# Performance work log

Measured on AMD Instinct MI355X. Metric: run time of the kernel, lower is better.

Reference implementation:

```python
import jax, jax.numpy as jnp
import numpy as np

N_NODES = 50000
N_EDGES = 600000
IN_FEAT = 128
EDGE_DIM = 3
N_HEADS = 4
OUT_FEAT = 32  # per head; N_HEADS*OUT_FEAT == IN_FEAT -> residual_proj is Identity


def setup_inputs() -> dict:
    key = jax.random.key(0)
    ks = jax.random.split(key, 16)
    s = 0.05
    H, F = N_HEADS, OUT_FEAT
    return {
        "node_feats": jax.random.normal(ks[0], (N_NODES, IN_FEAT), jnp.float32),
        "edge_feat": jax.random.normal(ks[1], (N_EDGES, EDGE_DIM), jnp.float32),
        "src": jax.random.randint(ks[2], (N_EDGES,), 0, N_NODES),
        "dst": jax.random.randint(ks[3], (N_EDGES,), 0, N_NODES),
        "W_em1": jax.random.normal(ks[4], (EDGE_DIM, 2 * EDGE_DIM), jnp.float32) * s,
        "b_em1": jnp.zeros((2 * EDGE_DIM,), jnp.float32),
        "W_em2": jax.random.normal(ks[5], (2 * EDGE_DIM, EDGE_DIM), jnp.float32) * s,
        "b_em2": jnp.zeros((EDGE_DIM,), jnp.float32),
        "W_np": jax.random.normal(ks[6], (IN_FEAT, IN_FEAT), jnp.float32) * s,
        "b_np": jnp.zeros((IN_FEAT,), jnp.float32),
        "W_fc": jax.random.normal(ks[7], (IN_FEAT + EDGE_DIM, H * F), jnp.float32) * s,
        "attn_l": jax.random.normal(ks[8], (H, F), jnp.float32) * s,
        "attn_r": jax.random.normal(ks[9], (H, F), jnp.float32) * s,
        "gat_bias": jnp.zeros((H * F,), jnp.float32),
        "ln_gamma": jnp.ones((H * F,), jnp.float32),
        "ln_beta": jnp.zeros((H * F,), jnp.float32),
    }


def reference(node_feats, edge_feat, src, dst, W_em1, b_em1, W_em2, b_em2,
              W_np, b_np, W_fc, attn_l, attn_r, gat_bias, ln_gamma, ln_beta):
    N = node_feats.shape[0]
    H, F = attn_l.shape
    # edge MLP: Linear -> SiLU -> Linear
    e = jax.nn.silu(edge_feat @ W_em1 + b_em1) @ W_em2 + b_em2            # [E, ED]
    p = node_feats @ W_np + b_np                                          # [N, IN]
    src_in = jnp.concatenate([p[src], e], axis=1)                         # [E, IN+ED]
    dst_in = jnp.concatenate([p[dst], e], axis=1)                         # [E, IN+ED]
    temp = jnp.zeros((N, src_in.shape[1]), node_feats.dtype)
    temp = temp.at[src].add(src_in).at[dst].add(dst_in)                   # scatter_add x2
    # GATConv (eval mode: feat_drop/attn_drop are identity)
    h = (temp @ W_fc).reshape(N, H, F)                                    # [N, H, F]
    el = jnp.einsum('nhf,hf->nh', h, attn_l)                              # [N, H]
    er = jnp.einsum('nhf,hf->nh', h, attn_r)                              # [N, H]
    logits = jax.nn.leaky_relu(el[src] + er[dst], negative_slope=0.2)     # [E, H]
    # destination-wise edge softmax (stable)
    m = jax.ops.segment_max(logits, dst, num_segments=N)                  # [N, H]
    a = jnp.exp(logits - m[dst])                                          # [E, H]
    z = jax.ops.segment_sum(a, dst, num_segments=N)                       # [N, H]
    alpha = a / z[dst]                                                    # [E, H]
    msg = alpha[:, :, None] * h[src]                                      # [E, H, F]
    rst = jax.ops.segment_sum(msg, dst, num_segments=N)                   # [N, H, F]
    rst = rst + gat_bias.reshape(1, H, F)
    gat_out = rst.reshape(N, H * F)
    out = gat_out + node_feats                                            # residual (Identity proj)
    mu = out.mean(axis=-1, keepdims=True)
    var = out.var(axis=-1, keepdims=True)
    out = (out - mu) / jnp.sqrt(var + 1e-5) * ln_gamma + ln_beta          # LayerNorm
    return jax.nn.silu(out)
```

## Files before the change

kernel.cpp:

```cpp
#include <hip/hip_runtime.h>
#include <hip/hip_bf16.h>

#define IN_FEAT 128
#define N_HEADS 4
#define OUT_FEAT 32

typedef __attribute__((ext_vector_type(8))) short short8;
typedef __attribute__((ext_vector_type(4))) float floatx4;

__device__ __forceinline__ void bf16split(float x, short& hi, short& lo) {
    unsigned u = __float_as_uint(x);
    unsigned r = (u + 0x7FFFu + ((u >> 16) & 1u)) & 0xFFFF0000u;
    hi = (short)(r >> 16);
    float res = x - __uint_as_float(r);
    unsigned u2 = __float_as_uint(res);
    unsigned r2 = u2 + 0x7FFFu + ((u2 >> 16) & 1u);
    lo = (short)(r2 >> 16);
}

__device__ __forceinline__ unsigned short bf16rne(float x) {
    unsigned u = __float_as_uint(x);
    return (unsigned short)((u + 0x7FFFu + ((u >> 16) & 1u)) >> 16);
}

__global__ void edge_scatter_kernel(const float* __restrict__ ef,
                                    const int* __restrict__ src, const int* __restrict__ dst,
                                    const float* __restrict__ W1, const float* __restrict__ b1,
                                    const float* __restrict__ W2, const float* __restrict__ b2,
                                    float* __restrict__ nd, int* __restrict__ erank, int E) {
    int t = blockIdx.x * blockDim.x + threadIdx.x;
    int e = t >> 3;
    int sub = t & 7;
    if (e >= E) return;
    float x0 = ef[e * 3 + 0], x1 = ef[e * 3 + 1], x2 = ef[e * 3 + 2];
    float hbuf[6];
#pragma unroll
    for (int j = 0; j < 6; j++) {
        float v = x0 * W1[0 * 6 + j] + x1 * W1[1 * 6 + j] + x2 * W1[2 * 6 + j] + b1[j];
        hbuf[j] = v / (1.0f + __expf(-v));
    }
    int j = sub & 3;
    float val;
    if (j == 0) {
        val = 1.0f;
    } else {
        float v = b2[j - 1];
#pragma unroll
        for (int k = 0; k < 6; k++) v += hbuf[k] * W2[k * 3 + (j - 1)];
        val = v;
    }
    int side = sub >> 2;
    int node = side ? dst[e] : src[e];
    int slot = (side && j == 0) ? 4 : j;
    float old = atomicAdd(&nd[(size_t)node * 8 + slot], val);
    if (sub == 4) erank[e] = (int)old;
}

__global__ __launch_bounds__(1024) void scan1_kernel(const float* __restrict__ nd,
                                                     int* __restrict__ excl,
                                                     int* __restrict__ bsum, int N) {
    __shared__ int buf[1024];
    int t = threadIdx.x;
    int i = blockIdx.x * 1024 + t;
    int v = (i < N) ? (int)nd[(size_t)i * 8 + 4] : 0;
    buf[t] = v;
    __syncthreads();
    for (int d = 1; d < 1024; d <<= 1) {
        int x = (t >= d) ? buf[t - d] : 0;
        __syncthreads();
        buf[t] += x;
        __syncthreads();
    }
    if (i < N) excl[i] = buf[t] - v;
    if (t == 1023) bsum[blockIdx.x] = buf[1023];
}

__global__ __launch_bounds__(1024) void scan2_kernel(const int* __restrict__ bsum,
                                                     int* __restrict__ boff, int nb) {
    __shared__ int buf[1024];
    int t = threadIdx.x;
    int v = (t < nb) ? bsum[t] : 0;
    buf[t] = v;
    __syncthreads();
    for (int d = 1; d < 1024; d <<= 1) {
        int x = (t >= d) ? buf[t - d] : 0;
        __syncthreads();
        buf[t] += x;
        __syncthreads();
    }
    if (t < nb) boff[t] = buf[t] - v;
}

__global__ __launch_bounds__(1024) void scan3_kernel(const int* __restrict__ excl,
                                                     const int* __restrict__ boff,
                                                     int* __restrict__ off, int N, int E) {
    int i = blockIdx.x * 1024 + threadIdx.x;
    if (i < N) off[i] = excl[i] + boff[blockIdx.x];
    if (i == 0) off[N] = E;
}

__global__ void bin_kernel(const int* __restrict__ src, const int* __restrict__ dst,
                           const int* __restrict__ eoff, const int* __restrict__ erank,
                           int* __restrict__ sorted_src, int E) {
    int e = blockIdx.x * blockDim.x + threadIdx.x;
    if (e >= E) return;
    sorted_src[eoff[dst[e]] + erank[e]] = src[e];
}

__global__ void wcomb_kernel(const float* __restrict__ W_np, const float* __restrict__ W_fc,
                             const float* __restrict__ b_np,
                             short* __restrict__ WBh, short* __restrict__ WBl,
                             float* __restrict__ bvec) {
    int i = blockIdx.x;
    int o = threadIdx.x;
    float acc = 0.0f;
    for (int j = 0; j < 128; j++) acc += W_np[i * 128 + j] * W_fc[j * 128 + o];
    short hi, lo;
    bf16split(acc, hi, lo);
    int t    = o >> 4;
    int kk   = i >> 5;
    int lane = ((i >> 3) & 3) * 16 + (o & 15);
    int jj   = i & 7;
    int fi = ((t * 4 + kk) * 64 + lane) * 8 + jj;
    WBh[fi] = hi;
    WBl[fi] = lo;
    if (i == 0) {
        float bb = 0.0f;
        for (int j = 0; j < 128; j++) bb += b_np[j] * W_fc[j * 128 + o];
        bvec[o] = bb;
    }
}

__global__ __launch_bounds__(256) void node_h_mfma_kernel(
        const float* __restrict__ nf,
        const short* __restrict__ WBh, const short* __restrict__ WBl,
        const float* __restrict__ bvec, const float* __restrict__ W_fc,
        const float* __restrict__ nd,
        const float* __restrict__ attn_l, const float* __restrict__ attn_r,
        unsigned short* __restrict__ h16,
        float* __restrict__ el, float* __restrict__ er, int N) {
    __shared__ short lWh[16384];
    __shared__ short lWl[16384];
    {
        const int4* s1 = (const int4*)WBh;
        const int4* s2 = (const int4*)WBl;
        int4* d1 = (int4*)lWh;
        int4* d2 = (int4*)lWl;
        for (int i = threadIdx.x; i < 2048; i += 256) { d1[i] = s1[i]; d2[i] = s2[i]; }
    }
    __syncthreads();

    const int w = threadIdx.x >> 6, l = threadIdx.x & 63;
    const int lrow = l & 15, lhalf = l >> 4;
    const int n0 = blockIdx.x * 64 + w * 16;
    const int arow = n0 + lrow;

    short8 ah[4], al_[4];
#pragma unroll
    for (int kk = 0; kk < 4; kk++) {
        float v[8];
        if (arow < N) {
            const float* p = &nf[(size_t)arow * 128 + kk * 32 + lhalf * 8];
            float4 f0 = *(const float4*)p;
            float4 f1 = *(const float4*)(p + 4);
            v[0] = f0.x; v[1] = f0.y; v[2] = f0.z; v[3] = f0.w;
            v[4] = f1.x; v[5] = f1.y; v[6] = f1.z; v[7] = f1.w;
        } else {
#pragma unroll
            for (int j = 0; j < 8; j++) v[j] = 0.0f;
        }
#pragma unroll
        for (int j = 0; j < 8; j++) {
            short hi, lo;
            bf16split(v[j], hi, lo);
            ah[kk][j] = hi;
            al_[kk][j] = lo;
        }
    }

    floatx4 acc[8];
#pragma unroll
    for (int t = 0; t < 8; t++) acc[t] = (floatx4){0.f, 0.f, 0.f, 0.f};

#pragma unroll
    for (int t = 0; t < 8; t++) {
#pragma unroll
        for (int kk = 0; kk < 4; kk++) {
            int fi = ((t * 4 + kk) * 64 + l) * 8;
            short8 bh = *(const short8*)&lWh[fi];
            short8 bl = *(const short8*)&lWl[fi];
            acc[t] = __builtin_amdgcn_mfma_f32_16x16x32_bf16(ah[kk], bh, acc[t], 0, 0, 0);
            acc[t] = __builtin_amdgcn_mfma_f32_16x16x32_bf16(ah[kk], bl, acc[t], 0, 0, 0);
            acc[t] = __builtin_amdgcn_mfma_f32_16x16x32_bf16(al_[kk], bh, acc[t], 0, 0, 0);
        }
    }

    float bv[8], w0[8], w1[8], w2[8], alb[8], arb[8];
#pragma unroll
    for (int t = 0; t < 8; t++) {
        int o = t * 16 + lrow;
        bv[t] = bvec[o];
        w0[t] = W_fc[128 * 128 + o];
        w1[t] = W_fc[129 * 128 + o];
        w2[t] = W_fc[130 * 128 + o];
        alb[t] = attn_l[o];
        arb[t] = attn_r[o];
    }
#pragma unroll
    for (int r = 0; r < 4; r++) {
        int node = n0 + lhalf * 4 + r;
        bool valid = node < N;
        float dg = 0.f, e0 = 0.f, e1 = 0.f, e2 = 0.f;
        if (valid) {
            dg = nd[(size_t)node * 8 + 0] + nd[(size_t)node * 8 + 4];
            e0 = nd[(size_t)node * 8 + 1];
            e1 = nd[(size_t)node * 8 + 2];
            e2 = nd[(size_t)node * 8 + 3];
        }
        float pl[4] = {0.f, 0.f, 0.f, 0.f}, pr[4] = {0.f, 0.f, 0.f, 0.f};
#pragma unroll
        for (int t = 0; t < 8; t++) {
            float hv = dg * (acc[t][r] + bv[t]) + e0 * w0[t] + e1 * w1[t] + e2 * w2[t];
            if (valid) h16[(size_t)node * 128 + t * 16 + lrow] = bf16rne(hv);
            pl[t >> 1] += hv * alb[t];
            pr[t >> 1] += hv * arb[t];
        }
#pragma unroll
        for (int hd = 0; hd < 4; hd++) {
#pragma unroll
            for (int mask = 1; mask <= 8; mask <<= 1) {
                pl[hd] += __shfl_xor(pl[hd], mask);
                pr[hd] += __shfl_xor(pr[hd], mask);
            }
        }
        if (valid) {
            if (lrow < 4)      el[node * 4 + lrow]       = pl[lrow];
            else if (lrow < 8) er[node * 4 + (lrow - 4)] = pr[lrow - 4];
        }
    }
}

__global__ __launch_bounds__(256) void gather_kernel(
        const int* __restrict__ off, const int* __restrict__ sorted_src,
        const float* __restrict__ el, const float* __restrict__ er,
        const unsigned short* __restrict__ h16, const float* __restrict__ nf,
        const float* __restrict__ gat_bias, const float* __restrict__ gamma,
        const float* __restrict__ beta, float* __restrict__ out, int N) {
    int n = (blockIdx.x * blockDim.x + threadIdx.x) >> 6;
    int lane = threadIdx.x & 63;
    if (n >= N) return;
    int o0 = lane * 2;
    int hd = lane >> 4;
    float ern = er[n * 4 + hd];
    int beg = off[n], end = off[n + 1];
    float z = 0.f, a0 = 0.f, a1 = 0.f;
    if (beg < end) {
        int s = sorted_src[beg];
        float elv = el[s * 4 + hd];
        unsigned hb = *(const unsigned*)&h16[(size_t)s * 128 + o0];
        for (int j = beg; j < end; j++) {
            int s2 = (j + 1 < end) ? sorted_src[j + 1] : s;
            float elv2 = el[s2 * 4 + hd];
            unsigned hb2 = *(const unsigned*)&h16[(size_t)s2 * 128 + o0];
            float l = elv + ern;
            l = (l > 0.f) ? l : 0.2f * l;
            float p = __expf(l);
            float hv0 = __uint_as_float(hb << 16);
            float hv1 = __uint_as_float(hb & 0xFFFF0000u);
            z  += p;
            a0 += p * hv0;
            a1 += p * hv1;
            elv = elv2; hb = hb2; s = s2;
        }
    }
    float r0 = (end > beg) ? a0 / z : 0.f;
    float r1 = (end > beg) ? a1 / z : 0.f;
    float2 nfv = *(const float2*)&nf[(size_t)n * 128 + o0];
    float v0 = r0 + gat_bias[o0]     + nfv.x;
    float v1 = r1 + gat_bias[o0 + 1] + nfv.y;
    float s = v0 + v1, s2 = v0 * v0 + v1 * v1;
#pragma unroll
    for (int mask = 32; mask; mask >>= 1) {
        s  += __shfl_xor(s, mask);
        s2 += __shfl_xor(s2, mask);
    }
    float mu = s * (1.0f / 128.0f);
    float var = s2 * (1.0f / 128.0f) - mu * mu;
    float inv = rsqrtf(var + 1e-5f);
    float y0 = (v0 - mu) * inv * gamma[o0]     + beta[o0];
    float y1 = (v1 - mu) * inv * gamma[o0 + 1] + beta[o0 + 1];
    float2 ov;
    ov.x = y0 / (1.0f + __expf(-y0));
    ov.y = y1 / (1.0f + __expf(-y1));
    *(float2*)&out[(size_t)n * 128 + o0] = ov;
}

extern "C" void kernel_launch(void* const* d_in, const int* in_sizes, int n_in,
                              void* d_out, int out_size, void* d_ws, size_t ws_size,
                              hipStream_t stream) {
    const float* nf     = (const float*)d_in[0];
    const float* ef     = (const float*)d_in[1];
    const int*   src    = (const int*)d_in[2];
    const int*   dst    = (const int*)d_in[3];
    const float* W_em1  = (const float*)d_in[4];
    const float* b_em1  = (const float*)d_in[5];
    const float* W_em2  = (const float*)d_in[6];
    const float* b_em2  = (const float*)d_in[7];
    const float* W_np   = (const float*)d_in[8];
    const float* b_np   = (const float*)d_in[9];
    const float* W_fc   = (const float*)d_in[10];
    const float* attn_l = (const float*)d_in[11];
    const float* attn_r = (const float*)d_in[12];
    const float* g_bias = (const float*)d_in[13];
    const float* ln_g   = (const float*)d_in[14];
    const float* ln_b   = (const float*)d_in[15];

    const int N = in_sizes[0] / IN_FEAT;
    const int E = in_sizes[2];

    float* ws = (float*)d_ws;
    size_t off_w = 0;
    auto alloc = [&](size_t nelem) {
        float* p = ws + off_w;
        off_w += (nelem + 63) & ~(size_t)63;
        return p;
    };
    float* nd    = alloc((size_t)N * 8);
    short* WBh   = (short*)alloc(128 * 128 / 2);
    short* WBl   = (short*)alloc(128 * 128 / 2);
    float* bvec  = alloc(128);
    unsigned short* h16 = (unsigned short*)alloc((size_t)N * 64);
    float* el    = alloc((size_t)N * 4);
    float* er    = alloc((size_t)N * 4);
    int*   erank  = (int*)alloc(E);
    int*   eoff   = (int*)alloc(N + 1);
    int*   ssrc   = (int*)alloc(E);
    int*   excl   = (int*)alloc(N);
    int*   bsum   = (int*)alloc(1024);
    int*   boff   = (int*)alloc(1024);

    const int nb = (N + 1023) / 1024;

    hipMemsetAsync(nd, 0, (size_t)N * 8 * sizeof(float), stream);

    edge_scatter_kernel<<<((size_t)E * 8 + 255) / 256, 256, 0, stream>>>(
        ef, src, dst, W_em1, b_em1, W_em2, b_em2, nd, erank, E);
    scan1_kernel<<<nb, 1024, 0, stream>>>(nd, excl, bsum, N);
    scan2_kernel<<<1, 1024, 0, stream>>>(bsum, boff, nb);
    scan3_kernel<<<nb, 1024, 0, stream>>>(excl, boff, eoff, N, E);
    bin_kernel<<<(E + 255) / 256, 256, 0, stream>>>(src, dst, eoff, erank, ssrc, E);
    wcomb_kernel<<<128, 128, 0, stream>>>(W_np, W_fc, b_np, WBh, WBl, bvec);
    node_h_mfma_kernel<<<(N + 63) / 64, 256, 0, stream>>>(nf, WBh, WBl, bvec, W_fc, nd,
                                                          attn_l, attn_r, h16, el, er, N);
    gather_kernel<<<((size_t)N * 64 + 255) / 256, 256, 0, stream>>>(eoff, ssrc, el, er, h16, nf,
                                                                    g_bias, ln_g, ln_b,
                                                                    (float*)d_out, N);
}
```

Before: 171.4 us.

## Fuse edge binning into node projection kernel and deepen gather prefetch

Removes the standalone bin kernel and folds the edge binning into the node MFMA kernel with a grid-stride loop. This cuts one launch and lets the scatter traffic overlap with the MFMA work. The wcomb launch is moved earlier so it no longer sits between scan and the fused kernel. The gather loop now prefetches two edges ahead instead of one, giving more memory-level parallelism at the cost of extra registers. The fused kernel also does scatter work before its MFMA phase, which may lengthen the time each block holds its large LDS allocation.

```diff
diff --git a/kernel.cpp b/kernel.cpp
--- a/kernel.cpp
+++ b/kernel.cpp
@@ -97,14 +97,6 @@
     int i = blockIdx.x * 1024 + threadIdx.x;
     if (i < N) off[i] = excl[i] + boff[blockIdx.x];
     if (i == 0) off[N] = E;
-}
-
-__global__ void bin_kernel(const int* __restrict__ src, const int* __restrict__ dst,
-                           const int* __restrict__ eoff, const int* __restrict__ erank,
-                           int* __restrict__ sorted_src, int E) {
-    int e = blockIdx.x * blockDim.x + threadIdx.x;
-    if (e >= E) return;
-    sorted_src[eoff[dst[e]] + erank[e]] = src[e];
 }
 
 __global__ void wcomb_kernel(const float* __restrict__ W_np, const float* __restrict__ W_fc,
@@ -131,7 +123,10 @@
     }
 }
 
-__global__ __launch_bounds__(256) void node_h_mfma_kernel(
+__global__ __launch_bounds__(256) void binh_kernel(
+        const int* __restrict__ src, const int* __restrict__ dst,
+        const int* __restrict__ eoff, const int* __restrict__ erank,
+        int* __restrict__ ssrc, int E,
         const float* __restrict__ nf,
         const short* __restrict__ WBh, const short* __restrict__ WBl,
         const float* __restrict__ bvec, const float* __restrict__ W_fc,
@@ -150,6 +145,14 @@
     }
     __syncthreads();
 
+    {
+        int stride = gridDim.x * 256;
+#pragma unroll 4
+        for (int e = blockIdx.x * 256 + threadIdx.x; e < E; e += stride) {
+            ssrc[eoff[dst[e]] + erank[e]] = src[e];
+        }
+    }
+
     const int w = threadIdx.x >> 6, l = threadIdx.x & 63;
     const int lrow = l & 15, lhalf = l >> 4;
     const int n0 = blockIdx.x * 64 + w * 16;
@@ -255,22 +258,24 @@
     int beg = off[n], end = off[n + 1];
     float z = 0.f, a0 = 0.f, a1 = 0.f;
     if (beg < end) {
-        int s = sorted_src[beg];
-        float elv = el[s * 4 + hd];
-        unsigned hb = *(const unsigned*)&h16[(size_t)s * 128 + o0];
+        int sA = sorted_src[beg];
+        int sB = (beg + 1 < end) ? sorted_src[beg + 1] : sA;
+        float elA = el[sA * 4 + hd];
+        float elB = el[sB * 4 + hd];
+        unsigned hbA = *(const unsigned*)&h16[(size_t)sA * 128 + o0];
+        unsigned hbB = *(const unsigned*)&h16[(size_t)sB * 128 + o0];
         for (int j = beg; j < end; j++) {
-            int s2 = (j + 1 < end) ? sorted_src[j + 1] : s;
-            float elv2 = el[s2 * 4 + hd];
-            unsigned hb2 = *(const unsigned*)&h16[(size_t)s2 * 128 + o0];
-            float l = elv + ern;
+            int sC = (j + 2 < end) ? sorted_src[j + 2] : sA;
+            float elC = el[sC * 4 + hd];
+            unsigned hbC = *(const unsigned*)&h16[(size_t)sC * 128 + o0];
+            float l = elA + ern;
             l = (l > 0.f) ? l : 0.2f * l;
             float p = __expf(l);
-            float hv0 = __uint_as_float(hb << 16);
-            float hv1 = __uint_as_float(hb & 0xFFFF0000u);
             z  += p;
-            a0 += p * hv0;
-            a1 += p * hv1;
-            elv = elv2; hb = hb2; s = s2;
+            a0 += p * __uint_as_float(hbA << 16);
+            a1 += p * __uint_as_float(hbA & 0xFFFF0000u);
+            elA = elB; hbA = hbB;
+            elB = elC; hbB = hbC;
         }
     }
     float r0 = (end > beg) ? a0 / z : 0.f;
@@ -345,13 +350,13 @@
 
     edge_scatter_kernel<<<((size_t)E * 8 + 255) / 256, 256, 0, stream>>>(
         ef, src, dst, W_em1, b_em1, W_em2, b_em2, nd, erank, E);
+    wcomb_kernel<<<128, 128, 0, stream>>>(W_np, W_fc, b_np, WBh, WBl, bvec);
     scan1_kernel<<<nb, 1024, 0, stream>>>(nd, excl, bsum, N);
     scan2_kernel<<<1, 1024, 0, stream>>>(bsum, boff, nb);
     scan3_kernel<<<nb, 1024, 0, stream>>>(excl, boff, eoff, N, E);
-    bin_kernel<<<(E + 255) / 256, 256, 0, stream>>>(src, dst, eoff, erank, ssrc, E);
-    wcomb_kernel<<<128, 128, 0, stream>>>(W_np, W_fc, b_np, WBh, WBl, bvec);
-    node_h_mfma_kernel<<<(N + 63) / 64, 256, 0, stream>>>(nf, WBh, WBl, bvec, W_fc, nd,
-                                                          attn_l, attn_r, h16, el, er, N);
+    binh_kernel<<<(N + 63) / 64, 256, 0, stream>>>(src, dst, eoff, erank, ssrc, E,
+                                                   nf, WBh, WBl, bvec, W_fc, nd,
+                                                   attn_l, attn_r, h16, el, er, N);
     gather_kernel<<<((size_t)N * 64 + 255) / 256, 256, 0, stream>>>(eoff, ssrc, el, er, h16, nf,
                                                                     g_bias, ln_g, ln_b,
                                                                     (float*)d_out, N);
```

Measured after the change: 171.4 us. About the same (+0.0%).
